# Kernel optimization log

Hardware: AMD Instinct MI355X
Metric: run time of the kernel (lower is better)

## Reference

```python
import jax, jax.numpy as jnp
import numpy as np

N, FIN, H, O, K = 300000, 128, 64, 32, 5


def setup_inputs() -> dict:
    key = jax.random.key(0)
    ks = jax.random.split(key, 8)
    xav_uh = (2.0 / (FIN + H)) ** 0.5  # xavier_normal scale for Linear(FIN, H)
    xav_ho = (2.0 / (H + O)) ** 0.5
    return {
        "user": jax.random.normal(ks[0], (N, FIN), dtype=jnp.float32),
        "item": jax.random.normal(ks[1], (N, FIN), dtype=jnp.float32),
        "r": jax.random.randint(ks[2], (N,), 0, K),
        "c": jax.random.uniform(ks[3], (N,), dtype=jnp.float32),
        # relation-stacked Linear weights, torch layout [out, in] -> [K, H, FIN]
        "Wu": jax.random.normal(ks[4], (K, H, FIN), dtype=jnp.float32) * xav_uh,
        "bu": jnp.zeros((K, H), dtype=jnp.float32),
        "Wv": jax.random.normal(ks[5], (K, H, FIN), dtype=jnp.float32) * xav_uh,
        "bv": jnp.zeros((K, H), dtype=jnp.float32),
        "Wl": jax.random.normal(ks[6], (O, H), dtype=jnp.float32) * xav_ho,
        "bl": jnp.zeros((O,), dtype=jnp.float32),
    }


def reference(user, item, r, c, Wu, bu, Wv, bv, Wl, bl):
    # Per-row relation-indexed linear: out[i] = x[i] @ W[r[i]].T + b[r[i]]
    def rel_linear(x, W, b):
        allp = jnp.einsum("ni,khi->nkh", x, W) + b[None]  # [N, K, H]
        return jnp.take_along_axis(allp, r[:, None, None], axis=1)[:, 0, :]  # [N, H]

    u_next = c[:, None] * rel_linear(item, Wu, bu)  # messages from items to users
    v_next = c[:, None] * rel_linear(user, Wv, bv)  # messages from users to items
    u_out = jax.nn.relu(jax.nn.relu(u_next) @ Wl.T + bl)
    v_out = jax.nn.relu(jax.nn.relu(v_next) @ Wl.T + bl)
    return (u_out, v_out)
```

## Files before the change

### kernel.cpp

```cpp
#include <hip/hip_runtime.h>
#include <hip/hip_bf16.h>

#define N_ROWS 300000
#define FIN    128
#define HDIM   64
#define ODIM   32
#define KREL   5
#define BR     64
#define NTILES ((N_ROWS + BR - 1) / BR + KREL)
#define NB     (NTILES * BR)
#define TPB    8
#define MAXCHUNK ((NTILES + TPB - 1) / TPB + KREL)
#define NBH    ((N_ROWS + 255) / 256)

typedef __attribute__((ext_vector_type(8))) short bf8_t;
typedef __attribute__((ext_vector_type(4))) float f32x4;
typedef __attribute__((ext_vector_type(4))) unsigned int u32x4;

static __device__ __forceinline__ unsigned pk2(float lo, float hi) {
  __hip_bfloat162 h = __float22bfloat162_rn(make_float2(lo, hi));
  return *reinterpret_cast<unsigned*>(&h);
}

static __device__ __forceinline__ bf8_t cvt8(float4 a, float4 b) {
  u32x4 u;
  u.x = pk2(a.x, a.y);
  u.y = pk2(a.z, a.w);
  u.z = pk2(b.x, b.y);
  u.w = pk2(b.z, b.w);
  return __builtin_bit_cast(bf8_t, u);
}

static __device__ __forceinline__ void stbf4_pk(void* base, int byte, float4 v) {
  unsigned long long p = (unsigned long long)pk2(v.x, v.y)
                       | ((unsigned long long)pk2(v.z, v.w) << 32);
  *(unsigned long long*)((char*)base + byte) = p;
}

static __device__ __forceinline__ bf8_t lds_load16(const void* base, int byte) {
  return *(const bf8_t*)((const char*)base + byte);
}

__global__ void blockhist_kernel(const int* __restrict__ r, int* __restrict__ blockcnt) {
  __shared__ int lc[KREL];
  int tid = threadIdx.x;
  if (tid < KREL) lc[tid] = 0;
  __syncthreads();
  int i = blockIdx.x * 256 + tid;
  if (i < N_ROWS) atomicAdd(&lc[r[i]], 1);
  __syncthreads();
  if (tid < KREL) blockcnt[blockIdx.x * KREL + tid] = lc[tid];
}

__global__ void scan_kernel(const int* __restrict__ blockcnt, int* __restrict__ base,
                            int* __restrict__ aoff, int* __restrict__ cb,
                            int* __restrict__ ts) {
  __shared__ int totals[KREL];
  __shared__ int aoff_s[KREL + 1];
  const int tid  = threadIdx.x;
  const int k    = tid >> 6;
  const int lane = tid & 63;

  if (k < KREL) {
    int part = 0;
    for (int b = lane; b < NBH; b += 64) part += blockcnt[b * KREL + k];
    #pragma unroll
    for (int off = 1; off < 64; off <<= 1) part += __shfl_xor(part, off);
    if (lane == 0) totals[k] = part;
  }
  __syncthreads();

  if (tid == 0) {
    int off = 0, cc = 0;
    for (int kk = 0; kk < KREL; ++kk) {
      aoff[kk] = off; aoff_s[kk] = off;
      off += ((totals[kk] + BR - 1) / BR) * BR;
    }
    aoff[KREL] = off; aoff_s[KREL] = off;
    for (int kk = 0; kk < KREL; ++kk) {
      ts[kk] = aoff_s[kk] / BR;
      int ntk = (aoff_s[kk + 1] - aoff_s[kk]) / BR;
      cb[kk] = cc;
      cc += (ntk + TPB - 1) / TPB;
    }
    cb[KREL] = cc;
    ts[KREL] = aoff_s[KREL] / BR;
  }
  __syncthreads();

  if (k < KREL) {
    int running = aoff_s[k];
    for (int b0 = 0; b0 < NBH; b0 += 64) {
      int b = b0 + lane;
      int v = (b < NBH) ? blockcnt[b * KREL + k] : 0;
      int s = v;
      #pragma unroll
      for (int off = 1; off < 64; off <<= 1) {
        int t = __shfl_up(s, off);
        if (lane >= off) s += t;
      }
      if (b < NBH) base[b * KREL + k] = running + s - v;
      running += __shfl(s, 63);
    }
  }
}

__global__ void scatter2_kernel(const int* __restrict__ r, const float* __restrict__ c,
                                const int* __restrict__ base, int* __restrict__ bucket,
                                float* __restrict__ cbv) {
  __shared__ int wcnt[4][KREL];
  __shared__ int wbase[4][KREL];
  const int tid  = threadIdx.x;
  const int wid  = tid >> 6;
  const int lane = tid & 63;
  const int i = blockIdx.x * 256 + tid;
  int k = -1; float cv = 0.f;
  if (i < N_ROWS) { k = r[i]; cv = c[i]; }

  int rank = 0;
  #pragma unroll
  for (int kk = 0; kk < KREL; ++kk) {
    unsigned long long m = __ballot(k == kk);
    if (lane == 0) wcnt[wid][kk] = __popcll(m);
    if (k == kk) rank = __popcll(m & ((1ull << lane) - 1ull));
  }
  __syncthreads();
  if (tid < KREL) {
    int b = base[blockIdx.x * KREL + tid];
    #pragma unroll
    for (int w = 0; w < 4; ++w) { wbase[w][tid] = b; b += wcnt[w][tid]; }
  }
  __syncthreads();
  if (i >= 0 && i < N_ROWS) {
    int pos = wbase[wid][k] + rank;
    bucket[pos] = i;
    cbv[pos]    = cv;
  }
}


__global__ __launch_bounds__(256, 3) void gcn_main(
    const float* __restrict__ user, const float* __restrict__ item,
    const float* __restrict__ Wu, const float* __restrict__ bu,
    const float* __restrict__ Wv, const float* __restrict__ bv,
    const float* __restrict__ Wl, const float* __restrict__ bl,
    const int* __restrict__ bucket, const float* __restrict__ cbv,
    const int* __restrict__ cb, const int* __restrict__ ts,
    float* __restrict__ out)
{
  __shared__ __align__(16) unsigned short sW[HDIM * FIN];
  __shared__ __align__(16) unsigned short sX[2][BR * FIN];

  const int tid  = threadIdx.x;
  const int side = blockIdx.x & 1;
  const int cid  = blockIdx.x >> 1;
  if (cid >= cb[KREL]) return;

  const int rel = (cid >= cb[1]) + (cid >= cb[2]) + (cid >= cb[3]) + (cid >= cb[4]);
  const int t_begin = ts[rel] + (cid - cb[rel]) * TPB;
  const int t_end   = (t_begin + TPB < ts[rel + 1]) ? t_begin + TPB : ts[rel + 1];

  const float* X  = side ? user : item;
  const float* Wk = side ? Wv : Wu;
  const float* bk = side ? bv : bu;

  const int lane = tid & 63;
  const int wid  = tid >> 6;
  const int lrow = lane & 15;
  const int lkg  = lane >> 4;
  const int sh   = lane >> 5;
  const int c4   = lane & 31;

  {
    const float4* w4 = (const float4*)(Wk + (size_t)rel * HDIM * FIN);
    #pragma unroll
    for (int it = 0; it < 8; ++it) {
      int f4  = it * 256 + tid;
      int row = f4 >> 5;
      int cc  = f4 & 31;
      int byte = (row * 256 + cc * 8) ^ ((row & 7) << 4);
      stbf4_pk(sW, byte, w4[f4]);
    }
  }

  bf8_t wl[2][2];
  #pragma unroll
  for (int n2 = 0; n2 < 2; ++n2)
    #pragma unroll
    for (int k2 = 0; k2 < 2; ++k2) {
      const float* p = Wl + (size_t)(n2 * 16 + lrow) * HDIM + k2 * 32 + lkg * 8;
      wl[n2][k2] = cvt8(*(const float4*)p, *(const float4*)(p + 4));
    }
  const float blv0 = bl[lrow];
  const float blv1 = bl[16 + lrow];
  float bfrag[4];
  #pragma unroll
  for (int n = 0; n < 4; ++n) bfrag[n] = bk[rel * HDIM + n * 16 + lrow];

  int idxA[8], idxB[8];
  {
    const int tB = (t_begin + 1 < t_end) ? t_begin + 1 : t_begin;
    #pragma unroll
    for (int it = 0; it < 8; ++it) {
      idxA[it] = bucket[t_begin * BR + wid * 16 + it * 2 + sh];
      idxB[it] = bucket[tB * BR + wid * 16 + it * 2 + sh];
    }
  }

  {
    char* myX0 = (char*)sX[0] + wid * 4096;
    #pragma unroll
    for (int it = 0; it < 8; ++it) {
      int idx  = idxA[it] < 0 ? 0 : idxA[it];
      float4 a = *(const float4*)(X + (size_t)idx * FIN + c4 * 4);
      int rl   = it * 2 + sh;
      int byte = (rl * 256 + c4 * 8) ^ ((rl & 7) << 4);
      stbf4_pk(myX0, byte, a);
    }
  }
  __syncthreads();

  for (int t = t_begin; t < t_end; ++t) {
    const int pb = (t - t_begin) & 1;
    char* myX = (char*)sX[pb] + wid * 4096;
    char* nX  = (char*)sX[pb ^ 1] + wid * 4096;
    const int tile0 = t * BR;
    const bool do_stage = (t + 1 < t_end);

    int idxC[8];
    {
      const int tC = (t + 2 < t_end) ? t + 2 : t;
      #pragma unroll
      for (int it = 0; it < 8; ++it)
        idxC[it] = bucket[tC * BR + wid * 16 + it * 2 + sh];
    }

    float4 ld[8];
    if (do_stage) {
      #pragma unroll
      for (int it = 0; it < 8; ++it) {
        int idx = idxB[it] < 0 ? 0 : idxB[it];
        ld[it]  = *(const float4*)(X + (size_t)idx * FIN + c4 * 4);
      }
    }

    const int erow = tile0 + wid * 16 + lkg * 4;
    int4   idxQ4 = *(const int4*)(bucket + erow);
    float4 cQ4   = *(const float4*)(cbv + erow);
    int   idxQ[4] = {idxQ4.x, idxQ4.y, idxQ4.z, idxQ4.w};
    float cQ[4]   = {cQ4.x, cQ4.y, cQ4.z, cQ4.w};

    __builtin_amdgcn_sched_barrier(0);

    f32x4 acc[4];
    #pragma unroll
    for (int n = 0; n < 4; ++n) acc[n] = f32x4{0.f, 0.f, 0.f, 0.f};

    const int axor = (lrow & 7) << 4;
    #pragma unroll
    for (int kc = 0; kc < 4; ++kc) {
      const int kb = (kc * 32 + lkg * 8) * 2;
      bf8_t au = lds_load16(myX, (lrow * 256 + kb) ^ axor);
      #pragma unroll
      for (int n = 0; n < 4; ++n) {
        int brow = n * 16 + lrow;
        int bx   = (brow * 256 + kb) ^ ((brow & 7) << 4);
        acc[n] = __builtin_amdgcn_mfma_f32_16x16x32_bf16(au, lds_load16(sW, bx), acc[n], 0, 0, 0);
      }
    }

    #pragma unroll
    for (int n = 0; n < 4; ++n) {
      int hcol = n * 16 + lrow;
      #pragma unroll
      for (int q = 0; q < 4; ++q) {
        int rr   = lkg * 4 + q;
        int byte = (rr * 128 + hcol * 2) ^ ((rr & 7) << 4);
        float hv = fmaxf(cQ[q] * (acc[n][q] + bfrag[n]), 0.f);
        *(unsigned short*)(myX + byte) = (unsigned short)(pk2(hv, hv) & 0xFFFFu);
      }
    }

    f32x4 acc2[2];
    acc2[0] = f32x4{0.f, 0.f, 0.f, 0.f};
    acc2[1] = f32x4{0.f, 0.f, 0.f, 0.f};
    #pragma unroll
    for (int k2 = 0; k2 < 2; ++k2) {
      const int kb = (k2 * 32 + lkg * 8) * 2;
      const int ax = (lrow * 128 + kb) ^ axor;
      bf8_t a2 = lds_load16(myX, ax);
      #pragma unroll
      for (int n2 = 0; n2 < 2; ++n2)
        acc2[n2] = __builtin_amdgcn_mfma_f32_16x16x32_bf16(a2, wl[n2][k2], acc2[n2], 0, 0, 0);
    }

    const size_t obase = (size_t)side * N_ROWS * ODIM;
    #pragma unroll
    for (int n2 = 0; n2 < 2; ++n2) {
      int col  = n2 * 16 + lrow;
      float bb = (n2 == 0) ? blv0 : blv1;
      #pragma unroll
      for (int q = 0; q < 4; ++q) {
        int idx = idxQ[q];
        if (idx >= 0)
          out[obase + (size_t)idx * ODIM + col] = fmaxf(acc2[n2][q] + bb, 0.f);
      }
    }

    __builtin_amdgcn_sched_barrier(0);

    if (do_stage) {
      #pragma unroll
      for (int it = 0; it < 8; ++it) {
        int rl   = it * 2 + sh;
        int byte = (rl * 256 + c4 * 8) ^ ((rl & 7) << 4);
        stbf4_pk(nX, byte, ld[it]);
      }
    }

    #pragma unroll
    for (int it = 0; it < 8; ++it) idxB[it] = idxC[it];
  }
}

extern "C" void kernel_launch(void* const* d_in, const int* in_sizes, int n_in,
                              void* d_out, int out_size, void* d_ws, size_t ws_size,
                              hipStream_t stream) {
  const float* user = (const float*)d_in[0];
  const float* item = (const float*)d_in[1];
  const int*   r    = (const int*)d_in[2];
  const float* c    = (const float*)d_in[3];
  const float* Wu   = (const float*)d_in[4];
  const float* bu   = (const float*)d_in[5];
  const float* Wv   = (const float*)d_in[6];
  const float* bv   = (const float*)d_in[7];
  const float* Wl   = (const float*)d_in[8];
  const float* bl   = (const float*)d_in[9];
  float* out = (float*)d_out;

  int*   bucket   = (int*)d_ws;
  float* cbv      = (float*)(bucket + NB);
  int*   blockcnt = (int*)(cbv + NB);
  int*   base     = blockcnt + NBH * KREL;
  int*   aoff     = base + NBH * KREL;
  int*   cb       = aoff + KREL + 1;
  int*   tsarr    = cb + KREL + 1;

  hipMemsetAsync(bucket, 0xFF, (size_t)NB * sizeof(int), stream);
  hipMemsetAsync(cbv, 0, (size_t)NB * sizeof(float), stream);

  blockhist_kernel<<<NBH, 256, 0, stream>>>(r, blockcnt);
  scan_kernel<<<1, 320, 0, stream>>>(blockcnt, base, aoff, cb, tsarr);
  scatter2_kernel<<<NBH, 256, 0, stream>>>(r, c, base, bucket, cbv);
  gcn_main<<<2 * MAXCHUNK, 256, 0, stream>>>(user, item, Wu, bu, Wv, bv, Wl, bl,
                                             bucket, cbv, cb, tsarr, out);
}
```

Before: 117.5 us.

## Deepen gather prefetch to two tiles ahead using ping-pong register banks

The main loop now issues global gathers for tile t+2 while computing tile t, using two alternating register banks, so each load has a full extra tile of compute to hide latency. Before, the gather ran only one tile ahead. Bucket indices are likewise fetched three tiles ahead, and the loop body becomes a lambda called with swapped bank references on even and odd iterations. This adds 32 more live VGPRs for the second float4 bank, which may reduce occupancy or cause spills.

```diff
diff --git a/kernel.cpp b/kernel.cpp
--- a/kernel.cpp
+++ b/kernel.cpp
@@ -197,54 +197,60 @@
   #pragma unroll
   for (int n = 0; n < 4; ++n) bfrag[n] = bk[rel * HDIM + n * 16 + lrow];
 
-  int idxA[8], idxB[8];
+  const int rbase = wid * 16 + sh;
+
+  float4 bank0[8], bank1[8];
+  int    idxP[8], idxR[8];
+
   {
+    int iA[8], iB[8];
     const int tB = (t_begin + 1 < t_end) ? t_begin + 1 : t_begin;
+    const int tC = (t_begin + 2 < t_end) ? t_begin + 2 : t_begin;
     #pragma unroll
     for (int it = 0; it < 8; ++it) {
-      idxA[it] = bucket[t_begin * BR + wid * 16 + it * 2 + sh];
-      idxB[it] = bucket[tB * BR + wid * 16 + it * 2 + sh];
-    }
-  }
-
-  {
+      iA[it]   = bucket[t_begin * BR + rbase + it * 2];
+      iB[it]   = bucket[tB * BR + rbase + it * 2];
+      idxP[it] = bucket[tC * BR + rbase + it * 2];
+    }
     char* myX0 = (char*)sX[0] + wid * 4096;
     #pragma unroll
     for (int it = 0; it < 8; ++it) {
-      int idx  = idxA[it] < 0 ? 0 : idxA[it];
+      int idx  = iA[it] < 0 ? 0 : iA[it];
       float4 a = *(const float4*)(X + (size_t)idx * FIN + c4 * 4);
       int rl   = it * 2 + sh;
       int byte = (rl * 256 + c4 * 8) ^ ((rl & 7) << 4);
       stbf4_pk(myX0, byte, a);
     }
-  }
-  __syncthreads();
-
-  for (int t = t_begin; t < t_end; ++t) {
+    if (t_begin + 1 < t_end) {
+      #pragma unroll
+      for (int it = 0; it < 8; ++it) {
+        int idx   = iB[it] < 0 ? 0 : iB[it];
+        bank0[it] = *(const float4*)(X + (size_t)idx * FIN + c4 * 4);
+      }
+    }
+  }
+  __syncthreads();
+
+  auto do_tile = [&](int t, float4 (&wb)[8], float4 (&gb)[8],
+                     int (&ci)[8], int (&di)[8]) {
     const int pb = (t - t_begin) & 1;
     char* myX = (char*)sX[pb] + wid * 4096;
     char* nX  = (char*)sX[pb ^ 1] + wid * 4096;
-    const int tile0 = t * BR;
-    const bool do_stage = (t + 1 < t_end);
-
-    int idxC[8];
-    {
-      const int tC = (t + 2 < t_end) ? t + 2 : t;
-      #pragma unroll
-      for (int it = 0; it < 8; ++it)
-        idxC[it] = bucket[tC * BR + wid * 16 + it * 2 + sh];
-    }
-
-    float4 ld[8];
-    if (do_stage) {
+
+    const int tD = (t + 3 < t_end) ? t + 3 : t_end - 1;
+    #pragma unroll
+    for (int it = 0; it < 8; ++it)
+      di[it] = bucket[tD * BR + rbase + it * 2];
+
+    if (t + 2 < t_end) {
       #pragma unroll
       for (int it = 0; it < 8; ++it) {
-        int idx = idxB[it] < 0 ? 0 : idxB[it];
-        ld[it]  = *(const float4*)(X + (size_t)idx * FIN + c4 * 4);
-      }
-    }
-
-    const int erow = tile0 + wid * 16 + lkg * 4;
+        int idx = ci[it] < 0 ? 0 : ci[it];
+        gb[it]  = *(const float4*)(X + (size_t)idx * FIN + c4 * 4);
+      }
+    }
+
+    const int erow = t * BR + wid * 16 + lkg * 4;
     int4   idxQ4 = *(const int4*)(bucket + erow);
     float4 cQ4   = *(const float4*)(cbv + erow);
     int   idxQ[4] = {idxQ4.x, idxQ4.y, idxQ4.z, idxQ4.w};
@@ -309,17 +315,19 @@
 
     __builtin_amdgcn_sched_barrier(0);
 
-    if (do_stage) {
+    if (t + 1 < t_end) {
       #pragma unroll
       for (int it = 0; it < 8; ++it) {
         int rl   = it * 2 + sh;
         int byte = (rl * 256 + c4 * 8) ^ ((rl & 7) << 4);
-        stbf4_pk(nX, byte, ld[it]);
-      }
-    }
-
-    #pragma unroll
-    for (int it = 0; it < 8; ++it) idxB[it] = idxC[it];
+        stbf4_pk(nX, byte, wb[it]);
+      }
+    }
+  };
+
+  for (int t = t_begin; t < t_end; ++t) {
+    if (((t - t_begin) & 1) == 0) do_tile(t, bank0, bank1, idxP, idxR);
+    else                          do_tile(t, bank1, bank0, idxR, idxP);
   }
 }
 
```

Result: slower. 248.0 us (+111.1%).
